# Performance work log

Measured on AMD Instinct MI355X. Metric: run time of the kernel, lower is better.

The kernel has to match this reference:

```python
import jax, jax.numpy as jnp
import numpy as np

TAU = 2.0
V_TH = 1.0
V_RESET = 0.0
BN_EPS = 1e-5
SG_ALPHA = 2.0  # spikingjelly ATan surrogate default

@jax.custom_vjp
def spike_fn(x):
    return (x >= 0.0).astype(x.dtype)

def _spike_fwd(x):
    return spike_fn(x), x

def _spike_bwd(x, g):
    # ATan surrogate: alpha/2 / (1 + (pi/2*alpha*x)^2)
    sg = (SG_ALPHA / 2.0) / (1.0 + (jnp.pi / 2.0 * SG_ALPHA * x) ** 2)
    return (g * sg,)

spike_fn.defvjp(_spike_fwd, _spike_bwd)

def lif_multistep(x_seq):
    # x_seq: [T, B, C]; decay_input=False, hard reset, detach_reset=True
    def step(v, xt):
        v = v - (v - V_RESET) / TAU + xt
        s = spike_fn(v - V_TH)
        sd = jax.lax.stop_gradient(s)
        v = (1.0 - sd) * v + sd * V_RESET
        return v, s
    v0 = jnp.zeros_like(x_seq[0])
    _, s_seq = jax.lax.scan(step, v0, x_seq)
    return s_seq

def bn_eval(x, gamma, beta, mean, var):
    # x: [T, B, C], normalize over channel C (eval-mode BN)
    inv = gamma * jax.lax.rsqrt(var + BN_EPS)
    return x * inv + (beta - mean * inv)

def setup_inputs() -> dict:
    key = jax.random.key(0)
    ks = jax.random.split(key, 8)
    B, T, Cin, C, K = 64, 200, 80, 1024, 7
    x = jax.random.normal(ks[0], (B, T, Cin), dtype=jnp.float32)
    pw_w = jax.random.normal(ks[1], (C, Cin), dtype=jnp.float32) * (1.0 / np.sqrt(Cin))
    pw_b = jnp.zeros((C,), dtype=jnp.float32)
    dw_w = jax.random.normal(ks[2], (C, K), dtype=jnp.float32) * (1.0 / np.sqrt(K))
    dw_b = jnp.zeros((C,), dtype=jnp.float32)
    bn1_gamma = jnp.ones((C,), dtype=jnp.float32)
    bn1_beta = jnp.zeros((C,), dtype=jnp.float32)
    bn1_mean = jnp.zeros((C,), dtype=jnp.float32)
    bn1_var = jnp.ones((C,), dtype=jnp.float32)
    lin_w = jax.random.normal(ks[3], (C, C), dtype=jnp.float32) * (1.0 / np.sqrt(C))
    bn2_gamma = jnp.ones((C,), dtype=jnp.float32)
    bn2_beta = jnp.zeros((C,), dtype=jnp.float32)
    bn2_mean = jnp.zeros((C,), dtype=jnp.float32)
    bn2_var = jnp.ones((C,), dtype=jnp.float32)
    return dict(x=x, pw_w=pw_w, pw_b=pw_b, dw_w=dw_w, dw_b=dw_b,
                bn1_gamma=bn1_gamma, bn1_beta=bn1_beta, bn1_mean=bn1_mean, bn1_var=bn1_var,
                lin_w=lin_w,
                bn2_gamma=bn2_gamma, bn2_beta=bn2_beta, bn2_mean=bn2_mean, bn2_var=bn2_var)

def reference(x, pw_w, pw_b, dw_w, dw_b,
              bn1_gamma, bn1_beta, bn1_mean, bn1_var,
              lin_w,
              bn2_gamma, bn2_beta, bn2_mean, bn2_var):
    # x: [B, T, Cin] -> trans1 -> [B, Cin, T]
    h = jnp.transpose(x, (0, 2, 1))
    # pointwise conv1d (kernel 1): [B, Cin, T] -> [B, C, T]
    h = jnp.einsum('bct,oc->bot', h, pw_w) + pw_b[None, :, None]
    # depthwise conv1d, kernel 7, same padding
    C = dw_w.shape[0]
    h = jax.lax.conv_general_dilated(
        h, dw_w[:, None, :], window_strides=(1,), padding=[(3, 3)],
        feature_group_count=C, dimension_numbers=('NCH', 'OIH', 'NCH'))
    h = h + dw_b[None, :, None]
    # trans2: [B, C, T] -> [T, B, C]
    h = jnp.transpose(h, (2, 0, 1))
    h = bn_eval(h, bn1_gamma, bn1_beta, bn1_mean, bn1_var)
    h = lif_multistep(h)
    # dropout1: eval mode -> identity
    h_res = h
    h = jnp.einsum('tbc,oc->tbo', h, lin_w)  # Linear, no bias
    h = bn_eval(h, bn2_gamma, bn2_beta, bn2_mean, bn2_var)
    h = lif_multistep(h)
    # dropout2: eval mode -> identity
    return h + h_res  # [T, B, C]
```

## Files before the change

kernel.cpp:

```cpp
#include <hip/hip_runtime.h>
#include <hip/hip_bf16.h>
#include <stdint.h>

#define B_    64
#define T_    200
#define CIN_  80
#define C_    1024
#define M_    (B_ * T_)
#define BCEL  (B_ * C_)

typedef __attribute__((ext_vector_type(4))) float f32x4;
typedef __attribute__((ext_vector_type(8))) _Float16 f16x8;
typedef __attribute__((ext_vector_type(4))) unsigned int u32x4;

__global__ __launch_bounds__(256) void gemm_abt(
    const float* __restrict__ A, const float* __restrict__ Bm,
    const float* __restrict__ bias, float* __restrict__ C,
    int M, int N, int K) {
  __shared__ float As[16][64];
  __shared__ float Bs[16][64];
  const int tid = threadIdx.x;
  const int tx = tid & 15;
  const int ty = tid >> 4;
  const int m0 = blockIdx.x * 64;
  const int n0 = blockIdx.y * 64;
  const int lr = tid >> 2;
  const int lc = (tid & 3) * 4;

  float acc[4][4] = {{0.f,0.f,0.f,0.f},{0.f,0.f,0.f,0.f},
                     {0.f,0.f,0.f,0.f},{0.f,0.f,0.f,0.f}};
  const float* Aro = A + (size_t)(m0 + lr) * K + lc;
  const float* Bro = Bm + (size_t)(n0 + lr) * K + lc;

  float4 a4 = *(const float4*)(Aro);
  float4 b4 = *(const float4*)(Bro);

  for (int k0 = 0; k0 < K; k0 += 16) {
    __syncthreads();
    As[lc + 0][lr] = a4.x; As[lc + 1][lr] = a4.y;
    As[lc + 2][lr] = a4.z; As[lc + 3][lr] = a4.w;
    Bs[lc + 0][lr] = b4.x; Bs[lc + 1][lr] = b4.y;
    Bs[lc + 2][lr] = b4.z; Bs[lc + 3][lr] = b4.w;
    __syncthreads();
    if (k0 + 16 < K) {
      a4 = *(const float4*)(Aro + k0 + 16);
      b4 = *(const float4*)(Bro + k0 + 16);
    }
#pragma unroll
    for (int kk = 0; kk < 16; ++kk) {
      float4 av = *(const float4*)&As[kk][ty * 4];
      float4 bv = *(const float4*)&Bs[kk][tx * 4];
      acc[0][0] = fmaf(av.x, bv.x, acc[0][0]);
      acc[0][1] = fmaf(av.x, bv.y, acc[0][1]);
      acc[0][2] = fmaf(av.x, bv.z, acc[0][2]);
      acc[0][3] = fmaf(av.x, bv.w, acc[0][3]);
      acc[1][0] = fmaf(av.y, bv.x, acc[1][0]);
      acc[1][1] = fmaf(av.y, bv.y, acc[1][1]);
      acc[1][2] = fmaf(av.y, bv.z, acc[1][2]);
      acc[1][3] = fmaf(av.y, bv.w, acc[1][3]);
      acc[2][0] = fmaf(av.z, bv.x, acc[2][0]);
      acc[2][1] = fmaf(av.z, bv.y, acc[2][1]);
      acc[2][2] = fmaf(av.z, bv.z, acc[2][2]);
      acc[2][3] = fmaf(av.z, bv.w, acc[2][3]);
      acc[3][0] = fmaf(av.w, bv.x, acc[3][0]);
      acc[3][1] = fmaf(av.w, bv.y, acc[3][1]);
      acc[3][2] = fmaf(av.w, bv.z, acc[3][2]);
      acc[3][3] = fmaf(av.w, bv.w, acc[3][3]);
    }
  }

  float bj[4] = {0.f, 0.f, 0.f, 0.f};
  if (bias) {
#pragma unroll
    for (int j = 0; j < 4; ++j) bj[j] = bias[n0 + tx * 4 + j];
  }
#pragma unroll
  for (int i = 0; i < 4; ++i) {
    int m = m0 + ty * 4 + i;
    float4 o4;
    o4.x = acc[i][0] + bj[0];
    o4.y = acc[i][1] + bj[1];
    o4.z = acc[i][2] + bj[2];
    o4.w = acc[i][3] + bj[3];
    *(float4*)&C[(size_t)m * N + n0 + tx * 4] = o4;
  }
}

__global__ __launch_bounds__(256) void dw_bn_lif(
    const float* __restrict__ p, const float* __restrict__ dw_w,
    const float* __restrict__ dw_b, const float* __restrict__ gam,
    const float* __restrict__ bet, const float* __restrict__ mu,
    const float* __restrict__ var, ushort* __restrict__ s1) {
  int gid = blockIdx.x * blockDim.x + threadIdx.x;
  int b = gid >> 10;
  int o = gid & 1023;

  float w[7];
#pragma unroll
  for (int k = 0; k < 7; ++k) w[k] = dw_w[o * 7 + k];
  float db = dw_b[o];
  float inv = (float)((double)gam[o] / sqrt((double)var[o] + 1e-5));
  float add = (float)((double)bet[o] - (double)mu[o] * (double)inv);

  const float* pp = p + (size_t)b * T_ * C_ + o;
  float win[14];
  win[0] = 0.f; win[1] = 0.f; win[2] = 0.f;
#pragma unroll
  for (int i = 0; i < 11; ++i) win[3 + i] = pp[(size_t)i * C_];

  float v = 0.f;
  size_t obase = (size_t)b * C_ + o;
  for (int c = 0; c < T_ / 8; ++c) {
    int t0 = c * 8;
    float nx[8];
#pragma unroll
    for (int j = 0; j < 8; ++j) {
      int tn = t0 + 11 + j;
      nx[j] = (tn < T_) ? pp[(size_t)tn * C_] : 0.f;
    }
#pragma unroll
    for (int s = 0; s < 8; ++s) {
      float u = db;
#pragma unroll
      for (int k = 0; k < 7; ++k) u = fmaf(w[k], win[s + k], u);
      u = fmaf(u, inv, add);
      v = fmaf(0.5f, v, u);
      bool sp = (v - 1.0f) >= 0.0f;
      s1[obase + (size_t)(t0 + s) * BCEL] = sp ? (ushort)0x3C00 : (ushort)0;
      v = sp ? 0.0f : v;
    }
#pragma unroll
    for (int i = 0; i < 6; ++i) win[i] = win[i + 8];
#pragma unroll
    for (int j = 0; j < 8; ++j) win[6 + j] = nx[j];
  }
}

__global__ __launch_bounds__(256) void split_w(
    const float* __restrict__ w, ushort* __restrict__ w0,
    ushort* __restrict__ w1, int n) {
  int i = blockIdx.x * 256 + threadIdx.x;
  if (i >= n) return;
  float x = w[i];
  union { _Float16 h; ushort u; } h0, h1;
  h0.h = (_Float16)x;
  if (fabsf(x) < 6.1035156e-5f) h0.u = 0;
  float r = x - (float)h0.h;
  h1.h = (_Float16)(r * 2048.0f);
  w0[i] = h0.u;
  w1[i] = h1.u;
}

#define BM 128
#define BN 128
#define BKg 32

__global__ __launch_bounds__(256) void gemm_mfma2p(
    const ushort* __restrict__ A,
    const ushort* __restrict__ B0,
    const ushort* __restrict__ B1,
    float* __restrict__ Cout) {
  const int K = C_;
  const int N = C_;
  __shared__ __align__(16) ushort lds[2][3][BM * BKg];

  const int tid  = threadIdx.x;
  const int lane = tid & 63;
  const int wm = ((tid >> 6) >> 1) * 64;
  const int wn = ((tid >> 6) & 1) * 64;

  int lin = blockIdx.x;
  int qq = gridDim.x >> 3;
  int wg = (lin & 7) * qq + (lin >> 3);
  const int m0 = (wg >> 3) * BM;
  const int n0 = (wg & 7) * BN;

  const int r0 = tid >> 2, r1 = r0 + 64;
  const int kc = (tid & 3) * 8;
  const int ks = kc ^ (((tid >> 3) & 3) << 3);

  const int fr = lane & 15;
  const int k8 = (lane >> 4) * 8;
  const int k8s = k8 ^ (((fr >> 1) & 3) << 3);

  f32x4 acc[4][4] = {};

#define STAGE(bufi, kk0)                                                       \
  do {                                                                         \
    __builtin_amdgcn_global_load_lds(                                          \
        (const __attribute__((address_space(1))) uint32_t*)(A + (size_t)(m0 + r0) * K + (kk0) + ks),  \
        (__attribute__((address_space(3))) uint32_t*)&lds[bufi][0][tid * 8], 16, 0, 0);               \
    __builtin_amdgcn_global_load_lds(                                          \
        (const __attribute__((address_space(1))) uint32_t*)(A + (size_t)(m0 + r1) * K + (kk0) + ks),  \
        (__attribute__((address_space(3))) uint32_t*)&lds[bufi][0][(tid + 256) * 8], 16, 0, 0);       \
    __builtin_amdgcn_global_load_lds(                                          \
        (const __attribute__((address_space(1))) uint32_t*)(B0 + (size_t)(n0 + r0) * K + (kk0) + ks), \
        (__attribute__((address_space(3))) uint32_t*)&lds[bufi][1][tid * 8], 16, 0, 0);               \
    __builtin_amdgcn_global_load_lds(                                          \
        (const __attribute__((address_space(1))) uint32_t*)(B0 + (size_t)(n0 + r1) * K + (kk0) + ks), \
        (__attribute__((address_space(3))) uint32_t*)&lds[bufi][1][(tid + 256) * 8], 16, 0, 0);       \
    __builtin_amdgcn_global_load_lds(                                          \
        (const __attribute__((address_space(1))) uint32_t*)(B1 + (size_t)(n0 + r0) * K + (kk0) + ks), \
        (__attribute__((address_space(3))) uint32_t*)&lds[bufi][2][tid * 8], 16, 0, 0);               \
    __builtin_amdgcn_global_load_lds(                                          \
        (const __attribute__((address_space(1))) uint32_t*)(B1 + (size_t)(n0 + r1) * K + (kk0) + ks), \
        (__attribute__((address_space(3))) uint32_t*)&lds[bufi][2][(tid + 256) * 8], 16, 0, 0);       \
  } while (0)

  STAGE(0, 0);
  __syncthreads();

  int buf = 0;
  for (int k0 = 0; k0 < K; k0 += BKg) {
    union HU { f16x8 h; u32x4 u; };
    f16x8 af[4], a2f[4], b0f[4], b1f[4];
#pragma unroll
    for (int m = 0; m < 4; ++m) {
      HU t;
      t.h = *(const f16x8*)&lds[buf][0][(wm + m * 16 + fr) * BKg + k8s];
      af[m] = t.h;
      t.u &= 0x10001000u;
      a2f[m] = t.h;
    }
#pragma unroll
    for (int n = 0; n < 4; ++n) {
      b0f[n] = *(const f16x8*)&lds[buf][1][(wn + n * 16 + fr) * BKg + k8s];
      b1f[n] = *(const f16x8*)&lds[buf][2][(wn + n * 16 + fr) * BKg + k8s];
    }
    if (k0 + BKg < K) STAGE(buf ^ 1, k0 + BKg);
#pragma unroll
    for (int m = 0; m < 4; ++m)
#pragma unroll
      for (int n = 0; n < 4; ++n) {
        acc[m][n] = __builtin_amdgcn_mfma_f32_16x16x32_f16(
            af[m], b0f[n], acc[m][n], 0, 0, 0);
        acc[m][n] = __builtin_amdgcn_mfma_f32_16x16x32_f16(
            a2f[m], b1f[n], acc[m][n], 0, 0, 0);
      }
    __syncthreads();
    buf ^= 1;
  }
#undef STAGE

  const int ccol = lane & 15;
  const int crow = (lane >> 4) * 4;
#pragma unroll
  for (int m = 0; m < 4; ++m)
#pragma unroll
    for (int n = 0; n < 4; ++n)
#pragma unroll
      for (int j = 0; j < 4; ++j) {
        int row = m0 + wm + m * 16 + crow + j;
        int col = n0 + wn + n * 16 + ccol;
        Cout[(size_t)row * N + col] = acc[m][n][j];
      }
}

__global__ __launch_bounds__(256) void bn_lif_add(
    const float* __restrict__ y, const ushort* __restrict__ s1b,
    const float* __restrict__ gam, const float* __restrict__ bet,
    const float* __restrict__ mu, const float* __restrict__ var,
    float* __restrict__ out) {
  int gid = blockIdx.x * blockDim.x + threadIdx.x;
  int o = gid & 1023;

  float inv = (float)((double)gam[o] / sqrt((double)var[o] + 1e-5));
  float add = (float)((double)bet[o] - (double)mu[o] * (double)inv);

  float v = 0.f;
  size_t base = (size_t)gid;
  float yv[8]; ushort sv[8];
#pragma unroll
  for (int j = 0; j < 8; ++j) {
    yv[j] = y[base + (size_t)j * BCEL];
    sv[j] = s1b[base + (size_t)j * BCEL];
  }
  for (int c = 0; c < T_ / 8; ++c) {
    int t0 = c * 8;
    float yn[8] = {0,0,0,0,0,0,0,0}; ushort sn[8] = {0,0,0,0,0,0,0,0};
    if (c + 1 < T_ / 8) {
#pragma unroll
      for (int j = 0; j < 8; ++j) {
        size_t idx = base + (size_t)(t0 + 8 + j) * BCEL;
        yn[j] = y[idx];
        sn[j] = s1b[idx];
      }
    }
#pragma unroll
    for (int j = 0; j < 8; ++j) {
      float u = fmaf(yv[j], inv, add);
      v = fmaf(0.5f, v, u);
      bool sp = (v - 1.0f) >= 0.0f;
      float s1v = sv[j] ? 1.0f : 0.0f;
      out[base + (size_t)(t0 + j) * BCEL] = (sp ? 1.0f : 0.0f) + s1v;
      v = sp ? 0.0f : v;
    }
#pragma unroll
    for (int j = 0; j < 8; ++j) { yv[j] = yn[j]; sv[j] = sn[j]; }
  }
}

extern "C" void kernel_launch(void* const* d_in, const int* in_sizes, int n_in,
                              void* d_out, int out_size, void* d_ws,
                              size_t ws_size, hipStream_t stream) {
  const float* x     = (const float*)d_in[0];
  const float* pw_w  = (const float*)d_in[1];
  const float* pw_b  = (const float*)d_in[2];
  const float* dw_w  = (const float*)d_in[3];
  const float* dw_b  = (const float*)d_in[4];
  const float* bn1g  = (const float*)d_in[5];
  const float* bn1b  = (const float*)d_in[6];
  const float* bn1m  = (const float*)d_in[7];
  const float* bn1v  = (const float*)d_in[8];
  const float* lin_w = (const float*)d_in[9];
  const float* bn2g  = (const float*)d_in[10];
  const float* bn2b  = (const float*)d_in[11];
  const float* bn2m  = (const float*)d_in[12];
  const float* bn2v  = (const float*)d_in[13];

  char* wsb  = (char*)d_ws;
  char* outb = (char*)d_out;
  const size_t PB  = (size_t)M_ * C_ * 4;
  const size_t SBB = (size_t)M_ * C_ * 2;

  float* p = (float*)d_ws;

  const bool primary = ws_size >= PB + SBB;
  ushort* spikes = primary ? (ushort*)(wsb + PB) : (ushort*)d_out;
  ushort* w0  = primary ? (ushort*)outb : (ushort*)(wsb + SBB);
  ushort* w1s = w0 + (size_t)C_ * C_;
  ushort* Sgemm = primary ? spikes : (ushort*)d_ws;
  float* ybuf = primary ? (float*)d_ws : (float*)d_out;

  dim3 pw_grid(M_ / 64, C_ / 64);
  gemm_abt<<<pw_grid, 256, 0, stream>>>(x, pw_w, pw_b, p, M_, C_, CIN_);

  dw_bn_lif<<<BCEL / 256, 256, 0, stream>>>(p, dw_w, dw_b, bn1g, bn1b, bn1m,
                                            bn1v, spikes);

  if (!primary)
    hipMemcpyAsync(d_ws, d_out, SBB, hipMemcpyDeviceToDevice, stream);

  split_w<<<(C_ * C_ + 255) / 256, 256, 0, stream>>>(lin_w, w0, w1s, C_ * C_);

  gemm_mfma2p<<<(M_ / BM) * (C_ / BN), 256, 0, stream>>>(Sgemm, w0, w1s, ybuf);

  bn_lif_add<<<BCEL / 256, 256, 0, stream>>>(ybuf, Sgemm, bn2g, bn2b, bn2m,
                                             bn2v, (float*)d_out);
}
```

Before: 153.3 us.

## Load A fragments directly to registers and triple-buffer B in LDS

The spike-matrix GEMM now reads the A operand fragments straight from global memory into registers, double-buffered across steps, rather than staging them through LDS. The B0/B1 weight halves move to a three-slot LDS ring with loads issued two steps ahead. Each step waits with a partial vmcnt and a single barrier instead of a full syncthreads, which lets loads overlap with the MFMA work. The cost is more VGPR use and uncoalesced per-lane global loads for A, and correctness now depends on the hand-set waitcnt count matching the number of loads in flight.

```diff
diff --git a/kernel.cpp b/kernel.cpp
--- a/kernel.cpp
+++ b/kernel.cpp
@@ -154,15 +154,16 @@
 #define BM 128
 #define BN 128
 #define BKg 32
-
-__global__ __launch_bounds__(256) void gemm_mfma2p(
+#define NSTEP (C_ / BKg)
+
+__global__ __launch_bounds__(256) void gemm_mfma2c(
     const ushort* __restrict__ A,
     const ushort* __restrict__ B0,
     const ushort* __restrict__ B1,
     float* __restrict__ Cout) {
   const int K = C_;
   const int N = C_;
-  __shared__ __align__(16) ushort lds[2][3][BM * BKg];
+  __shared__ __align__(16) ushort lds[3][2][BN * BKg];
 
   const int tid  = threadIdx.x;
   const int lane = tid & 63;
@@ -183,64 +184,81 @@
   const int k8 = (lane >> 4) * 8;
   const int k8s = k8 ^ (((fr >> 1) & 3) << 3);
 
+  const ushort* Af = A + (size_t)(m0 + wm + fr) * K + k8;
+
   f32x4 acc[4][4] = {};
-
-#define STAGE(bufi, kk0)                                                       \
+  f16x8 af_a[4], af_b[4];
+
+#define BSTAGE(bufi, kk0)                                                      \
   do {                                                                         \
+    int kk_ = (kk0) < K ? (kk0) : 0;                                           \
     __builtin_amdgcn_global_load_lds(                                          \
-        (const __attribute__((address_space(1))) uint32_t*)(A + (size_t)(m0 + r0) * K + (kk0) + ks),  \
-        (__attribute__((address_space(3))) uint32_t*)&lds[bufi][0][tid * 8], 16, 0, 0);               \
+        (const __attribute__((address_space(1))) uint32_t*)(B0 + (size_t)(n0 + r0) * K + kk_ + ks),  \
+        (__attribute__((address_space(3))) uint32_t*)&lds[bufi][0][tid * 8], 16, 0, 0);              \
     __builtin_amdgcn_global_load_lds(                                          \
-        (const __attribute__((address_space(1))) uint32_t*)(A + (size_t)(m0 + r1) * K + (kk0) + ks),  \
-        (__attribute__((address_space(3))) uint32_t*)&lds[bufi][0][(tid + 256) * 8], 16, 0, 0);       \
+        (const __attribute__((address_space(1))) uint32_t*)(B0 + (size_t)(n0 + r1) * K + kk_ + ks),  \
+        (__attribute__((address_space(3))) uint32_t*)&lds[bufi][0][(tid + 256) * 8], 16, 0, 0);      \
     __builtin_amdgcn_global_load_lds(                                          \
-        (const __attribute__((address_space(1))) uint32_t*)(B0 + (size_t)(n0 + r0) * K + (kk0) + ks), \
-        (__attribute__((address_space(3))) uint32_t*)&lds[bufi][1][tid * 8], 16, 0, 0);               \
+        (const __attribute__((address_space(1))) uint32_t*)(B1 + (size_t)(n0 + r0) * K + kk_ + ks),  \
+        (__attribute__((address_space(3))) uint32_t*)&lds[bufi][1][tid * 8], 16, 0, 0);              \
     __builtin_amdgcn_global_load_lds(                                          \
-        (const __attribute__((address_space(1))) uint32_t*)(B0 + (size_t)(n0 + r1) * K + (kk0) + ks), \
-        (__attribute__((address_space(3))) uint32_t*)&lds[bufi][1][(tid + 256) * 8], 16, 0, 0);       \
-    __builtin_amdgcn_global_load_lds(                                          \
-        (const __attribute__((address_space(1))) uint32_t*)(B1 + (size_t)(n0 + r0) * K + (kk0) + ks), \
-        (__attribute__((address_space(3))) uint32_t*)&lds[bufi][2][tid * 8], 16, 0, 0);               \
-    __builtin_amdgcn_global_load_lds(                                          \
-        (const __attribute__((address_space(1))) uint32_t*)(B1 + (size_t)(n0 + r1) * K + (kk0) + ks), \
-        (__attribute__((address_space(3))) uint32_t*)&lds[bufi][2][(tid + 256) * 8], 16, 0, 0);       \
+        (const __attribute__((address_space(1))) uint32_t*)(B1 + (size_t)(n0 + r1) * K + kk_ + ks),  \
+        (__attribute__((address_space(3))) uint32_t*)&lds[bufi][1][(tid + 256) * 8], 16, 0, 0);      \
   } while (0)
 
-  STAGE(0, 0);
-  __syncthreads();
-
-  int buf = 0;
-  for (int k0 = 0; k0 < K; k0 += BKg) {
-    union HU { f16x8 h; u32x4 u; };
-    f16x8 af[4], a2f[4], b0f[4], b1f[4];
-#pragma unroll
-    for (int m = 0; m < 4; ++m) {
-      HU t;
-      t.h = *(const f16x8*)&lds[buf][0][(wm + m * 16 + fr) * BKg + k8s];
-      af[m] = t.h;
-      t.u &= 0x10001000u;
-      a2f[m] = t.h;
-    }
-#pragma unroll
-    for (int n = 0; n < 4; ++n) {
-      b0f[n] = *(const f16x8*)&lds[buf][1][(wn + n * 16 + fr) * BKg + k8s];
-      b1f[n] = *(const f16x8*)&lds[buf][2][(wn + n * 16 + fr) * BKg + k8s];
-    }
-    if (k0 + BKg < K) STAGE(buf ^ 1, k0 + BKg);
-#pragma unroll
-    for (int m = 0; m < 4; ++m)
-#pragma unroll
-      for (int n = 0; n < 4; ++n) {
-        acc[m][n] = __builtin_amdgcn_mfma_f32_16x16x32_f16(
-            af[m], b0f[n], acc[m][n], 0, 0, 0);
-        acc[m][n] = __builtin_amdgcn_mfma_f32_16x16x32_f16(
-            a2f[m], b1f[n], acc[m][n], 0, 0, 0);
-      }
-    __syncthreads();
-    buf ^= 1;
-  }
-#undef STAGE
+#define ALOAD(dst, kk0)                                                        \
+  do {                                                                         \
+    int ka_ = (kk0) < K ? (kk0) : 0;                                           \
+    dst[0] = *(const f16x8*)(Af + (size_t)(0)  * K + ka_);                     \
+    dst[1] = *(const f16x8*)(Af + (size_t)(16) * K + ka_);                     \
+    dst[2] = *(const f16x8*)(Af + (size_t)(32) * K + ka_);                     \
+    dst[3] = *(const f16x8*)(Af + (size_t)(48) * K + ka_);                     \
+  } while (0)
+
+#define STEP(s, af_use, af_ld, bi_rd, bi_st)                                   \
+  do {                                                                         \
+    asm volatile("s_waitcnt vmcnt(8)" ::: "memory");                           \
+    __builtin_amdgcn_sched_barrier(0);                                         \
+    __builtin_amdgcn_s_barrier();                                              \
+    __builtin_amdgcn_sched_barrier(0);                                         \
+    f16x8 b0f[4], b1f[4];                                                      \
+    _Pragma("unroll")                                                          \
+    for (int n = 0; n < 4; ++n) {                                              \
+      b0f[n] = *(const f16x8*)&lds[bi_rd][0][(wn + n * 16 + fr) * BKg + k8s];  \
+      b1f[n] = *(const f16x8*)&lds[bi_rd][1][(wn + n * 16 + fr) * BKg + k8s];  \
+    }                                                                          \
+    ALOAD(af_ld, ((s) + 1) * BKg);                                             \
+    BSTAGE(bi_st, ((s) + 2) * BKg);                                            \
+    _Pragma("unroll")                                                          \
+    for (int m = 0; m < 4; ++m) {                                              \
+      union HU { f16x8 h; u32x4 u; } t, t2;                                    \
+      t.h = af_use[m];                                                         \
+      t2.u = t.u & 0x10001000u;          \
+      _Pragma("unroll")                                                        \
+      for (int n = 0; n < 4; ++n) {                                            \
+        acc[m][n] = __builtin_amdgcn_mfma_f32_16x16x32_f16(                    \
+            af_use[m], b0f[n], acc[m][n], 0, 0, 0);                            \
+        acc[m][n] = __builtin_amdgcn_mfma_f32_16x16x32_f16(                    \
+            t2.h, b1f[n], acc[m][n], 0, 0, 0);                                 \
+      }                                                                        \
+    }                                                                          \
+  } while (0)
+
+  BSTAGE(0, 0);
+  ALOAD(af_a, 0);
+  BSTAGE(1, BKg);
+
+  int bi0 = 0;
+  for (int s = 0; s < NSTEP; s += 2) {
+    int bi1 = bi0 + 1; if (bi1 == 3) bi1 = 0;
+    int bi2 = bi1 + 1; if (bi2 == 3) bi2 = 0;
+    STEP(s,     af_a, af_b, bi0, bi2);
+    STEP(s + 1, af_b, af_a, bi1, bi0);
+    bi0 = bi2;
+  }
+#undef STEP
+#undef ALOAD
+#undef BSTAGE
 
   const int ccol = lane & 15;
   const int crow = (lane >> 4) * 4;
@@ -343,7 +361,7 @@
 
   split_w<<<(C_ * C_ + 255) / 256, 256, 0, stream>>>(lin_w, w0, w1s, C_ * C_);
 
-  gemm_mfma2p<<<(M_ / BM) * (C_ / BN), 256, 0, stream>>>(Sgemm, w0, w1s, ybuf);
+  gemm_mfma2c<<<(M_ / BM) * (C_ / BN), 256, 0, stream>>>(Sgemm, w0, w1s, ybuf);
 
   bn_lif_add<<<BCEL / 256, 256, 0, stream>>>(ybuf, Sgemm, bn2g, bn2b, bn2m,
                                              bn2v, (float*)d_out);
```

Measured after the change: 165.2 us. 7.8% more time.

## Fuse pointwise conv GEMM into depthwise conv + BN + LIF kernel

Applied to the files above, without the earlier changes.

Replaces the separate FP32 pointwise GEMM and the depthwise/BN/LIF scan with one kernel. Each thread holds its channel's 80 pointwise weights in registers and computes the pointwise output per timestep from a double-buffered shared-memory tile of the input. A 7-tap sliding register window then feeds the depthwise conv and LIF directly. This removes the 52MB intermediate write and read plus one launch, at the cost of high register pressure and only 256 blocks doing a serial time loop.

```diff
diff --git a/kernel.cpp b/kernel.cpp
--- a/kernel.cpp
+++ b/kernel.cpp
@@ -13,127 +13,101 @@
 typedef __attribute__((ext_vector_type(8))) _Float16 f16x8;
 typedef __attribute__((ext_vector_type(4))) unsigned int u32x4;
 
-__global__ __launch_bounds__(256) void gemm_abt(
-    const float* __restrict__ A, const float* __restrict__ Bm,
-    const float* __restrict__ bias, float* __restrict__ C,
-    int M, int N, int K) {
-  __shared__ float As[16][64];
-  __shared__ float Bs[16][64];
-  const int tid = threadIdx.x;
-  const int tx = tid & 15;
-  const int ty = tid >> 4;
-  const int m0 = blockIdx.x * 64;
-  const int n0 = blockIdx.y * 64;
-  const int lr = tid >> 2;
-  const int lc = (tid & 3) * 4;
-
-  float acc[4][4] = {{0.f,0.f,0.f,0.f},{0.f,0.f,0.f,0.f},
-                     {0.f,0.f,0.f,0.f},{0.f,0.f,0.f,0.f}};
-  const float* Aro = A + (size_t)(m0 + lr) * K + lc;
-  const float* Bro = Bm + (size_t)(n0 + lr) * K + lc;
-
-  float4 a4 = *(const float4*)(Aro);
-  float4 b4 = *(const float4*)(Bro);
-
-  for (int k0 = 0; k0 < K; k0 += 16) {
-    __syncthreads();
-    As[lc + 0][lr] = a4.x; As[lc + 1][lr] = a4.y;
-    As[lc + 2][lr] = a4.z; As[lc + 3][lr] = a4.w;
-    Bs[lc + 0][lr] = b4.x; Bs[lc + 1][lr] = b4.y;
-    Bs[lc + 2][lr] = b4.z; Bs[lc + 3][lr] = b4.w;
-    __syncthreads();
-    if (k0 + 16 < K) {
-      a4 = *(const float4*)(Aro + k0 + 16);
-      b4 = *(const float4*)(Bro + k0 + 16);
-    }
-#pragma unroll
-    for (int kk = 0; kk < 16; ++kk) {
-      float4 av = *(const float4*)&As[kk][ty * 4];
-      float4 bv = *(const float4*)&Bs[kk][tx * 4];
-      acc[0][0] = fmaf(av.x, bv.x, acc[0][0]);
-      acc[0][1] = fmaf(av.x, bv.y, acc[0][1]);
-      acc[0][2] = fmaf(av.x, bv.z, acc[0][2]);
-      acc[0][3] = fmaf(av.x, bv.w, acc[0][3]);
-      acc[1][0] = fmaf(av.y, bv.x, acc[1][0]);
-      acc[1][1] = fmaf(av.y, bv.y, acc[1][1]);
-      acc[1][2] = fmaf(av.y, bv.z, acc[1][2]);
-      acc[1][3] = fmaf(av.y, bv.w, acc[1][3]);
-      acc[2][0] = fmaf(av.z, bv.x, acc[2][0]);
-      acc[2][1] = fmaf(av.z, bv.y, acc[2][1]);
-      acc[2][2] = fmaf(av.z, bv.z, acc[2][2]);
-      acc[2][3] = fmaf(av.z, bv.w, acc[2][3]);
-      acc[3][0] = fmaf(av.w, bv.x, acc[3][0]);
-      acc[3][1] = fmaf(av.w, bv.y, acc[3][1]);
-      acc[3][2] = fmaf(av.w, bv.z, acc[3][2]);
-      acc[3][3] = fmaf(av.w, bv.w, acc[3][3]);
-    }
-  }
-
-  float bj[4] = {0.f, 0.f, 0.f, 0.f};
-  if (bias) {
-#pragma unroll
-    for (int j = 0; j < 4; ++j) bj[j] = bias[n0 + tx * 4 + j];
-  }
-#pragma unroll
-  for (int i = 0; i < 4; ++i) {
-    int m = m0 + ty * 4 + i;
-    float4 o4;
-    o4.x = acc[i][0] + bj[0];
-    o4.y = acc[i][1] + bj[1];
-    o4.z = acc[i][2] + bj[2];
-    o4.w = acc[i][3] + bj[3];
-    *(float4*)&C[(size_t)m * N + n0 + tx * 4] = o4;
-  }
-}
-
-__global__ __launch_bounds__(256) void dw_bn_lif(
-    const float* __restrict__ p, const float* __restrict__ dw_w,
+#define CHT 8
+
+__global__ __launch_bounds__(256) void fused_pw_dw_lif(
+    const float* __restrict__ x, const float* __restrict__ pw_w,
+    const float* __restrict__ pw_b, const float* __restrict__ dw_w,
     const float* __restrict__ dw_b, const float* __restrict__ gam,
     const float* __restrict__ bet, const float* __restrict__ mu,
     const float* __restrict__ var, ushort* __restrict__ s1) {
-  int gid = blockIdx.x * blockDim.x + threadIdx.x;
-  int b = gid >> 10;
-  int o = gid & 1023;
-
-  float w[7];
-#pragma unroll
-  for (int k = 0; k < 7; ++k) w[k] = dw_w[o * 7 + k];
-  float db = dw_b[o];
-  float inv = (float)((double)gam[o] / sqrt((double)var[o] + 1e-5));
-  float add = (float)((double)bet[o] - (double)mu[o] * (double)inv);
-
-  const float* pp = p + (size_t)b * T_ * C_ + o;
-  float win[14];
-  win[0] = 0.f; win[1] = 0.f; win[2] = 0.f;
-#pragma unroll
-  for (int i = 0; i < 11; ++i) win[3 + i] = pp[(size_t)i * C_];
-
+  __shared__ __align__(16) float xs[2][CHT * CIN_];
+
+  const int tid = threadIdx.x;
+  const int b = blockIdx.x >> 2;
+  const int o = ((blockIdx.x & 3) << 8) | tid;
+
+  float w[CIN_];
+#pragma unroll
+  for (int k = 0; k < CIN_; k += 4) {
+    float4 q = *(const float4*)(pw_w + (size_t)o * CIN_ + k);
+    w[k] = q.x; w[k + 1] = q.y; w[k + 2] = q.z; w[k + 3] = q.w;
+  }
+  const float pb = pw_b[o];
+  const float d0 = dw_w[o * 7 + 0], d1 = dw_w[o * 7 + 1], d2 = dw_w[o * 7 + 2],
+              d3 = dw_w[o * 7 + 3], d4 = dw_w[o * 7 + 4], d5 = dw_w[o * 7 + 5],
+              d6 = dw_w[o * 7 + 6];
+  const float db = dw_b[o];
+  const float inv = (float)((double)gam[o] / sqrt((double)var[o] + 1e-5));
+  const float add = (float)((double)bet[o] - (double)mu[o] * (double)inv);
+
+  const float* xb_ = x + (size_t)b * T_ * CIN_;
+
+  {
+    float v0 = xb_[tid];
+    float v1 = xb_[tid + 256];
+    xs[0][tid] = v0;
+    xs[0][tid + 256] = v1;
+    if (tid < 128) xs[0][tid + 512] = xb_[tid + 512];
+  }
+  __syncthreads();
+
+  float r0 = 0.f, r1 = 0.f, r2 = 0.f, r3 = 0.f, r4 = 0.f, r5 = 0.f, r6 = 0.f;
   float v = 0.f;
-  size_t obase = (size_t)b * C_ + o;
-  for (int c = 0; c < T_ / 8; ++c) {
-    int t0 = c * 8;
-    float nx[8];
-#pragma unroll
-    for (int j = 0; j < 8; ++j) {
-      int tn = t0 + 11 + j;
-      nx[j] = (tn < T_) ? pp[(size_t)tn * C_] : 0.f;
-    }
-#pragma unroll
-    for (int s = 0; s < 8; ++s) {
-      float u = db;
-#pragma unroll
-      for (int k = 0; k < 7; ++k) u = fmaf(w[k], win[s + k], u);
-      u = fmaf(u, inv, add);
-      v = fmaf(0.5f, v, u);
-      bool sp = (v - 1.0f) >= 0.0f;
-      s1[obase + (size_t)(t0 + s) * BCEL] = sp ? (ushort)0x3C00 : (ushort)0;
-      v = sp ? 0.0f : v;
-    }
-#pragma unroll
-    for (int i = 0; i < 6; ++i) win[i] = win[i + 8];
-#pragma unroll
-    for (int j = 0; j < 8; ++j) win[6 + j] = nx[j];
-  }
+  const size_t obase = (size_t)b * C_ + o;
+
+#define EMIT_STEP(PT, TIDX)                                                    \
+  do {                                                                         \
+    r0 = r1; r1 = r2; r2 = r3; r3 = r4; r4 = r5; r5 = r6; r6 = (PT);           \
+    int t_ = (TIDX);                                                           \
+    if (t_ >= 0) {                                                             \
+      float u = db;                                                            \
+      u = fmaf(d0, r0, u); u = fmaf(d1, r1, u); u = fmaf(d2, r2, u);           \
+      u = fmaf(d3, r3, u); u = fmaf(d4, r4, u); u = fmaf(d5, r5, u);           \
+      u = fmaf(d6, r6, u);                                                     \
+      u = fmaf(u, inv, add);                                                   \
+      v = fmaf(0.5f, v, u);                                                    \
+      bool sp = (v - 1.0f) >= 0.0f;                                            \
+      s1[obase + (size_t)t_ * BCEL] = sp ? (ushort)0x3C00 : (ushort)0;         \
+      v = sp ? 0.0f : v;                                                       \
+    }                                                                          \
+  } while (0)
+
+  for (int c = 0; c < T_ / CHT; ++c) {
+    float p0 = 0.f, p1 = 0.f, p2 = 0.f;
+    if (c + 1 < T_ / CHT) {
+      const float* src = xb_ + (size_t)(c + 1) * (CHT * CIN_);
+      p0 = src[tid];
+      p1 = src[tid + 256];
+      if (tid < 128) p2 = src[tid + 512];
+    }
+    const float* rowb = &xs[c & 1][0];
+#pragma unroll
+    for (int s = 0; s < CHT; ++s) {
+      float acc = 0.f;
+#pragma unroll
+      for (int k4 = 0; k4 < CIN_ / 4; ++k4) {
+        float4 q = *(const float4*)(rowb + s * CIN_ + k4 * 4);
+        acc = fmaf(q.x, w[k4 * 4 + 0], acc);
+        acc = fmaf(q.y, w[k4 * 4 + 1], acc);
+        acc = fmaf(q.z, w[k4 * 4 + 2], acc);
+        acc = fmaf(q.w, w[k4 * 4 + 3], acc);
+      }
+      float pt = acc + pb;
+      EMIT_STEP(pt, c * CHT + s - 3);
+    }
+    __syncthreads();
+    if (c + 1 < T_ / CHT) {
+      xs[(c + 1) & 1][tid] = p0;
+      xs[(c + 1) & 1][tid + 256] = p1;
+      if (tid < 128) xs[(c + 1) & 1][tid + 512] = p2;
+    }
+    __syncthreads();
+  }
+  EMIT_STEP(0.f, 197);
+  EMIT_STEP(0.f, 198);
+  EMIT_STEP(0.f, 199);
+#undef EMIT_STEP
 }
 
 __global__ __launch_bounds__(256) void split_w(
@@ -323,8 +297,6 @@
   const size_t PB  = (size_t)M_ * C_ * 4;
   const size_t SBB = (size_t)M_ * C_ * 2;
 
-  float* p = (float*)d_ws;
-
   const bool primary = ws_size >= PB + SBB;
   ushort* spikes = primary ? (ushort*)(wsb + PB) : (ushort*)d_out;
   ushort* w0  = primary ? (ushort*)outb : (ushort*)(wsb + SBB);
@@ -332,11 +304,8 @@
   ushort* Sgemm = primary ? spikes : (ushort*)d_ws;
   float* ybuf = primary ? (float*)d_ws : (float*)d_out;
 
-  dim3 pw_grid(M_ / 64, C_ / 64);
-  gemm_abt<<<pw_grid, 256, 0, stream>>>(x, pw_w, pw_b, p, M_, C_, CIN_);
-
-  dw_bn_lif<<<BCEL / 256, 256, 0, stream>>>(p, dw_w, dw_b, bn1g, bn1b, bn1m,
-                                            bn1v, spikes);
+  fused_pw_dw_lif<<<BCEL / 256, 256, 0, stream>>>(
+      x, pw_w, pw_b, dw_w, dw_b, bn1g, bn1b, bn1m, bn1v, spikes);
 
   if (!primary)
     hipMemcpyAsync(d_ws, d_out, SBB, hipMemcpyDeviceToDevice, stream);
```

Measured after the change: 186.7 us. +21.8%, slower.
